# Kernel tuning notes

Measured on AMD Instinct MI355X. Metric: run time of the kernel, lower is better.

## Reference

```python
import jax, jax.numpy as jnp
import numpy as np

B, C, H, W = 4, 256, 64, 64
INTER = C // 2
BN_EPS = 1e-5


def setup_inputs() -> dict:
    key = jax.random.key(0)
    ks = jax.random.split(key, 12)
    s = 0.05
    return {
        "x": jax.random.normal(ks[0], (B, C, H, W), dtype=jnp.float32),
        "theta_w": jax.random.normal(ks[1], (INTER, C), dtype=jnp.float32) * s,
        "theta_b": jax.random.normal(ks[2], (INTER,), dtype=jnp.float32) * s,
        "phi_w": jax.random.normal(ks[3], (INTER, C), dtype=jnp.float32) * s,
        "phi_b": jax.random.normal(ks[4], (INTER,), dtype=jnp.float32) * s,
        "g_w": jax.random.normal(ks[5], (INTER, C), dtype=jnp.float32) * s,
        "g_b": jax.random.normal(ks[6], (INTER,), dtype=jnp.float32) * s,
        "W_w": jax.random.normal(ks[7], (C, INTER), dtype=jnp.float32) * s,
        "W_b": jax.random.normal(ks[8], (C,), dtype=jnp.float32) * s,
        "bn_gamma": jnp.ones((C,), dtype=jnp.float32),
        "bn_beta": jnp.zeros((C,), dtype=jnp.float32),
    }


def _conv1x1(x, w, b):
    # 1x1 conv == per-pixel GEMM: (B,C,H,W) x (O,C) -> (B,O,H,W)
    return jnp.einsum("bchw,oc->bohw", x, w) + b[None, :, None, None]


def reference(x, theta_w, theta_b, phi_w, phi_b, g_w, g_b, W_w, W_b, bn_gamma, bn_beta):
    b, c, h, w = x.shape
    hw = h * w
    theta = _conv1x1(x, theta_w, theta_b).reshape(b, -1, hw)  # (B, inter, HW) -> queries
    phi = _conv1x1(x, phi_w, phi_b).reshape(b, -1, hw)        # (B, inter, HW) -> keys
    g = _conv1x1(x, g_w, g_b).reshape(b, -1, hw)              # (B, inter, HW) -> values
    # f[n,m] = <theta[:,n], phi[:,m]> over all HW spatial positions
    f = jnp.einsum("bin,bim->bnm", theta, phi)                # (B, HW, HW)
    attn = jax.nn.softmax(f, axis=-1)
    y = jnp.einsum("bnm,bim->bin", attn, g)                   # (B, inter, HW)
    y = y.reshape(b, c // 2, h, w)
    wy = _conv1x1(y, W_w, W_b)                                # (B, C, H, W)
    # BatchNorm2d (training-mode batch statistics, per channel)
    mean = jnp.mean(wy, axis=(0, 2, 3), keepdims=True)
    var = jnp.var(wy, axis=(0, 2, 3), keepdims=True)
    wy_bn = bn_gamma[None, :, None, None] * (wy - mean) * jax.lax.rsqrt(var + BN_EPS) + bn_beta[None, :, None, None]
    return wy_bn + x
```

## Files before the change

kernel.cpp:

```cpp
#include <hip/hip_runtime.h>
#include <hip/hip_bf16.h>

#define HWN   4096
#define CIN   256
#define NINTER 128
#define NBATCH 4
#define BN_EPS 1e-5f
#define LOG2E 1.4426950408889634f
#define SMAX  64.0f

typedef __bf16 bf16_t;
typedef __bf16 bf16x8 __attribute__((ext_vector_type(8)));
typedef __bf16 bf16x4 __attribute__((ext_vector_type(4)));
typedef float  f32x4  __attribute__((ext_vector_type(4)));
typedef float  f32x16 __attribute__((ext_vector_type(16)));

__device__ __forceinline__ float fexp2(float x) {
  return __builtin_amdgcn_exp2f(x);
}

__device__ __forceinline__ void split_bf16(float v, bf16_t& h, bf16_t& l) {
  h = (bf16_t)v;
  l = (bf16_t)(v - (float)h);
}

__global__ __launch_bounds__(256) void convert_weights(
    const float* __restrict__ tw, const float* __restrict__ pw,
    const float* __restrict__ gw, const float* __restrict__ ww,
    bf16_t* __restrict__ out) {
  int i = blockIdx.x * 256 + threadIdx.x;
  float v;
  if (i < 32768)        v = tw[i];
  else if (i < 65536)   v = pw[i - 32768];
  else if (i < 98304)   v = gw[i - 65536];
  else                  v = ww[i - 98304];
  bf16_t h, l;
  split_bf16(v, h, l);
  out[i] = h;
  out[131072 + i] = l;
}

__global__ __launch_bounds__(256, 4) void qkv_kernel(
    const float* __restrict__ x, const bf16_t* __restrict__ wbf,
    const float* __restrict__ tb, const float* __restrict__ pb,
    const float* __restrict__ gb,
    bf16_t* __restrict__ Qh, bf16_t* __restrict__ Kh, bf16_t* __restrict__ V) {
  const int ntb  = blockIdx.x;
  const int b    = blockIdx.y;
  const int tid  = threadIdx.x;
  const int lane = tid & 63;
  const int wv   = tid >> 6;
  const int l31  = lane & 31;
  const int half = lane >> 5;

  __shared__ __align__(16) bf16_t smem[4608];
  bf16_t (*xTh)[72] = (bf16_t(*)[72])smem;
  bf16_t (*xTl)[72] = (bf16_t(*)[72])(smem + 2304);
  bf16_t (*Tr)[136] = (bf16_t(*)[136])smem;

  const bf16_t* Th = wbf;
  const bf16_t* Tl = wbf + 131072;
  const bf16_t* Ph = wbf + 32768;
  const bf16_t* Pl = wbf + 131072 + 32768;
  const bf16_t* Gh = wbf + 65536;
  const float*  xb = x + (size_t)b * CIN * HWN + ntb * 32;

  f32x16 aq, ak, av;
#pragma unroll
  for (int i = 0; i < 16; i++) { aq[i] = 0.f; ak[i] = 0.f; av[i] = 0.f; }

  for (int c0 = 0; c0 < 256; c0 += 64) {
    __syncthreads();
#pragma unroll
    for (int i = 0; i < 8; i++) {
      int idx = tid + i * 256;
      int cc = idx >> 5;
      int nn = idx & 31;
      float v = xb[(size_t)(c0 + cc) * HWN + nn];
      bf16_t h, l;
      split_bf16(v, h, l);
      xTh[nn][cc] = h;
      xTl[nn][cc] = l;
    }
    __syncthreads();
#pragma unroll
    for (int kk = 0; kk < 64; kk += 16) {
      size_t woff = (size_t)(32 * wv + l31) * 256 + c0 + kk + half * 8;
      bf16x8 th = *(const bf16x8*)(Th + woff);
      bf16x8 tl = *(const bf16x8*)(Tl + woff);
      bf16x8 ph = *(const bf16x8*)(Ph + woff);
      bf16x8 pl = *(const bf16x8*)(Pl + woff);
      bf16x8 gh = *(const bf16x8*)(Gh + woff);
      bf16x8 bh = *(const bf16x8*)(&xTh[l31][kk + half * 8]);
      bf16x8 bl = *(const bf16x8*)(&xTl[l31][kk + half * 8]);
      aq = __builtin_amdgcn_mfma_f32_32x32x16_bf16(th, bh, aq, 0, 0, 0);
      aq = __builtin_amdgcn_mfma_f32_32x32x16_bf16(th, bl, aq, 0, 0, 0);
      aq = __builtin_amdgcn_mfma_f32_32x32x16_bf16(tl, bh, aq, 0, 0, 0);
      ak = __builtin_amdgcn_mfma_f32_32x32x16_bf16(ph, bh, ak, 0, 0, 0);
      ak = __builtin_amdgcn_mfma_f32_32x32x16_bf16(ph, bl, ak, 0, 0, 0);
      ak = __builtin_amdgcn_mfma_f32_32x32x16_bf16(pl, bh, ak, 0, 0, 0);
      av = __builtin_amdgcn_mfma_f32_32x32x16_bf16(gh, bh, av, 0, 0, 0);
    }
  }

  const int trow = tid >> 3;
  const int tc16 = (tid & 7) * 16;
  bf16_t* qh = Qh + ((size_t)b * HWN + ntb * 32) * NINTER;
  bf16_t* kh = Kh + ((size_t)b * HWN + ntb * 32) * NINTER;

#pragma unroll
  for (int rnd = 0; rnd < 2; rnd++) {
    __syncthreads();
#pragma unroll
    for (int rg = 0; rg < 4; rg++) {
      int och0 = 32 * wv + 8 * rg + 4 * half;
#pragma unroll
      for (int j = 0; j < 4; j++) {
        float v = (rnd == 0) ? (aq[rg * 4 + j] + tb[och0 + j]) * LOG2E
                             : (ak[rg * 4 + j] + pb[och0 + j]);
        Tr[l31][och0 + j] = (bf16_t)v;
      }
    }
    __syncthreads();
    bf16_t* dst = (rnd == 0) ? qh : kh;
    bf16x8 v0 = *(const bf16x8*)(&Tr[trow][tc16]);
    bf16x8 v1 = *(const bf16x8*)(&Tr[trow][tc16 + 8]);
    *(bf16x8*)(dst + (size_t)trow * NINTER + tc16) = v0;
    *(bf16x8*)(dst + (size_t)trow * NINTER + tc16 + 8) = v1;
  }

  const int n = ntb * 32 + l31;
  bf16_t* vd = V + (size_t)b * NINTER * HWN;
#pragma unroll
  for (int r = 0; r < 16; r++) {
    int och = 32 * wv + (r & 3) + 8 * (r >> 2) + 4 * half;
    vd[(size_t)och * HWN + n] = (bf16_t)(av[r] + gb[och]);
  }
}

template<int NCv>
__global__ __launch_bounds__(256, 3) void attn_kernel(
    const bf16_t* __restrict__ Qh, const bf16_t* __restrict__ Kh,
    const bf16_t* __restrict__ V,
    float* __restrict__ Opart, float* __restrict__ Lp) {
  constexpr int CH = HWN / NCv;
  constexpr int NT = CH / 32;
  const int qt    = blockIdx.x;
  const int chunk = blockIdx.y;
  const int b     = blockIdx.z;
  const int tid   = threadIdx.x;
  const int lane  = tid & 63;
  const int wv    = tid >> 6;
  const int l15   = lane & 15;
  const int quad  = lane >> 4;
  const int kbase = chunk * CH;

  __shared__ __align__(16) bf16_t Klds[32][136];
  __shared__ __align__(16) bf16_t Vlds[144][56];
  __shared__ __align__(16) bf16_t Plds[4][32][40];

  const bf16_t* Qhb = Qh + (size_t)b * HWN * NINTER;
  const bf16_t* Khb = Kh + (size_t)b * HWN * NINTER;
  const bf16_t* Vb  = V + (size_t)b * NINTER * HWN;

  if (tid < 112) {
    int row = 128 + tid / 7;
    int c8 = (tid % 7) * 8;
    bf16x8 v;
#pragma unroll
    for (int j = 0; j < 8; j++) v[j] = (bf16_t)((row == 128) ? 1.0f : 0.0f);
    *(bf16x8*)(&Vlds[row][c8]) = v;
  }

  bf16x8 qf[2][4];
#pragma unroll
  for (int qs = 0; qs < 2; qs++) {
    const int qrow = qt * 128 + wv * 32 + qs * 16 + l15;
#pragma unroll
    for (int kc = 0; kc < 4; kc++)
      qf[qs][kc] = *(const bf16x8*)(Qhb + (size_t)qrow * NINTER + kc * 32 + quad * 8);
  }

  f32x4 o[2][8], ol[2];
#pragma unroll
  for (int qs = 0; qs < 2; qs++) {
#pragma unroll
    for (int dt = 0; dt < 8; dt++)
#pragma unroll
      for (int i = 0; i < 4; i++) o[qs][dt][i] = 0.f;
#pragma unroll
    for (int i = 0; i < 4; i++) ol[qs][i] = 0.f;
  }

  auto load_tile = [&](uint4* kr, uint4* vr, int t) {
#pragma unroll
    for (int i = 0; i < 2; i++) {
      int idx = tid + i * 256;
      kr[i] = *(const uint4*)(Khb + (size_t)(kbase + t * 32 + (idx >> 4)) * NINTER + (idx & 15) * 8);
    }
#pragma unroll
    for (int i = 0; i < 2; i++) {
      int idx = tid + i * 256;
      vr[i] = *(const uint4*)(Vb + (size_t)(idx >> 2) * HWN + kbase + t * 32 + (idx & 3) * 8);
    }
  };
  auto store_tile = [&](const uint4* kr, const uint4* vr) {
#pragma unroll
    for (int i = 0; i < 2; i++) {
      int idx = tid + i * 256;
      *(uint4*)(&Klds[idx >> 4][(idx & 15) * 8]) = kr[i];
    }
#pragma unroll
    for (int i = 0; i < 2; i++) {
      int idx = tid + i * 256;
      *(uint4*)(&Vlds[idx >> 2][(idx & 3) * 8]) = vr[i];
    }
  };

  auto compute = [&]() {
    f32x4 s[2][2];
#pragma unroll
    for (int qs = 0; qs < 2; qs++)
#pragma unroll
      for (int ks = 0; ks < 2; ks++)
#pragma unroll
        for (int i = 0; i < 4; i++) s[qs][ks][i] = 0.f;
#pragma unroll
    for (int ks = 0; ks < 2; ks++)
#pragma unroll
      for (int kc = 0; kc < 4; kc++) {
        bf16x8 kf = *(const bf16x8*)(&Klds[ks * 16 + l15][kc * 32 + quad * 8]);
        s[0][ks] = __builtin_amdgcn_mfma_f32_16x16x32_bf16(kf, qf[0][kc], s[0][ks], 0, 0, 0);
        s[1][ks] = __builtin_amdgcn_mfma_f32_16x16x32_bf16(kf, qf[1][kc], s[1][ks], 0, 0, 0);
      }

#pragma unroll
    for (int qs = 0; qs < 2; qs++)
#pragma unroll
      for (int ks = 0; ks < 2; ks++) {
        bf16x4 p4;
#pragma unroll
        for (int r = 0; r < 4; r++)
          p4[r] = (bf16_t)fexp2(s[qs][ks][r] - SMAX);
        *(bf16x4*)(&Plds[wv][qs * 16 + l15][ks * 16 + quad * 4]) = p4;
      }

    bf16x8 pf0 = *(const bf16x8*)(&Plds[wv][l15][quad * 8]);
    bf16x8 pf1 = *(const bf16x8*)(&Plds[wv][16 + l15][quad * 8]);
#pragma unroll
    for (int dt = 0; dt < 8; dt++) {
      bf16x8 vf = *(const bf16x8*)(&Vlds[dt * 16 + l15][quad * 8]);
      o[0][dt] = __builtin_amdgcn_mfma_f32_16x16x32_bf16(pf0, vf, o[0][dt], 0, 0, 0);
      o[1][dt] = __builtin_amdgcn_mfma_f32_16x16x32_bf16(pf1, vf, o[1][dt], 0, 0, 0);
    }
    bf16x8 vfl = *(const bf16x8*)(&Vlds[128 + l15][quad * 8]);
    ol[0] = __builtin_amdgcn_mfma_f32_16x16x32_bf16(pf0, vfl, ol[0], 0, 0, 0);
    ol[1] = __builtin_amdgcn_mfma_f32_16x16x32_bf16(pf1, vfl, ol[1], 0, 0, 0);
  };

  uint4 krA[2], vrA[2], krB[2], vrB[2];
  load_tile(krA, vrA, 0);

#pragma unroll 1
  for (int t = 0; t < NT; t += 2) {
    __builtin_amdgcn_s_barrier();
    __builtin_amdgcn_sched_barrier(0);
    store_tile(krA, vrA);
    __builtin_amdgcn_sched_barrier(0);
    load_tile(krB, vrB, t + 1);
    __builtin_amdgcn_sched_barrier(0);
    asm volatile("s_waitcnt lgkmcnt(0)" ::: "memory");
    __builtin_amdgcn_sched_barrier(0);
    __builtin_amdgcn_s_barrier();
    __builtin_amdgcn_sched_barrier(0);
    compute();

    __builtin_amdgcn_s_barrier();
    __builtin_amdgcn_sched_barrier(0);
    store_tile(krB, vrB);
    __builtin_amdgcn_sched_barrier(0);
    if (t + 2 < NT) load_tile(krA, vrA, t + 2);
    __builtin_amdgcn_sched_barrier(0);
    asm volatile("s_waitcnt lgkmcnt(0)" ::: "memory");
    __builtin_amdgcn_sched_barrier(0);
    __builtin_amdgcn_s_barrier();
    __builtin_amdgcn_sched_barrier(0);
    compute();
  }

  float* Ob = Opart + ((size_t)(b * NCv + chunk) * HWN) * NINTER;
#pragma unroll
  for (int qs = 0; qs < 2; qs++)
#pragma unroll
    for (int r = 0; r < 4; r++) {
      int n = qt * 128 + wv * 32 + qs * 16 + quad * 4 + r;
#pragma unroll
      for (int dt = 0; dt < 8; dt++)
        Ob[(size_t)n * NINTER + dt * 16 + l15] = o[qs][dt][r];
      if (l15 == 0)
        Lp[(size_t)(b * NCv + chunk) * HWN + n] = ol[qs][r];
    }
}

template<int NCv>
__global__ __launch_bounds__(256, 4) void wconv_kernel(
    const bf16_t* __restrict__ Wbf, const float* __restrict__ Opart,
    const float* __restrict__ Lp, const float* __restrict__ Wb,
    bf16_t* __restrict__ WY) {
  const int ntb = blockIdx.x;
  const int b   = blockIdx.y;
  const int tid = threadIdx.x;
  const int lane = tid & 63;
  const int wv   = tid >> 6;
  const int l31  = lane & 31;
  const int half = lane >> 5;

  __shared__ __align__(16) bf16_t Ylds[32][136];
  __shared__ float Linv[32];

  if (tid < 32) {
    int n = ntb * 32 + tid;
    float ls = 0.f;
#pragma unroll
    for (int c = 0; c < NCv; c++) ls += Lp[(size_t)(b * NCv + c) * HWN + n];
    Linv[tid] = 1.f / ls;
  }

  const int nrow = tid >> 3;
  const int dgrp = tid & 7;
  float oacc[16];
#pragma unroll
  for (int j = 0; j < 16; j++) oacc[j] = 0.f;
#pragma unroll
  for (int c = 0; c < NCv; c++) {
    const float* Op = Opart +
        ((size_t)(b * NCv + c) * HWN + ntb * 32 + nrow) * NINTER + dgrp * 16;
#pragma unroll
    for (int q = 0; q < 4; q++) {
      f32x4 v = *(const f32x4*)(Op + q * 4);
#pragma unroll
      for (int j = 0; j < 4; j++) oacc[q * 4 + j] += v[j];
    }
  }
  __syncthreads();
  {
    float inv = Linv[nrow];
    bf16x8 y0, y1;
#pragma unroll
    for (int j = 0; j < 8; j++) {
      y0[j] = (bf16_t)(oacc[j] * inv);
      y1[j] = (bf16_t)(oacc[8 + j] * inv);
    }
    *(bf16x8*)(&Ylds[nrow][dgrp * 16]) = y0;
    *(bf16x8*)(&Ylds[nrow][dgrp * 16 + 8]) = y1;
  }
  __syncthreads();

  const bf16_t* Wh = Wbf + 98304;
  f32x16 acc[2];
#pragma unroll
  for (int c = 0; c < 2; c++)
#pragma unroll
    for (int i = 0; i < 16; i++) acc[c][i] = 0.f;

#pragma unroll
  for (int k0 = 0; k0 < 128; k0 += 16) {
    bf16x8 a0 = *(const bf16x8*)(Wh + (size_t)(wv * 64 + l31) * NINTER + k0 + half * 8);
    bf16x8 a1 = *(const bf16x8*)(Wh + (size_t)(wv * 64 + 32 + l31) * NINTER + k0 + half * 8);
    bf16x8 b0 = *(const bf16x8*)(&Ylds[l31][k0 + half * 8]);
    acc[0] = __builtin_amdgcn_mfma_f32_32x32x16_bf16(a0, b0, acc[0], 0, 0, 0);
    acc[1] = __builtin_amdgcn_mfma_f32_32x32x16_bf16(a1, b0, acc[1], 0, 0, 0);
  }

  bf16_t* dst = WY + (size_t)b * 256 * HWN + ntb * 32;
#pragma unroll
  for (int ct = 0; ct < 2; ct++)
#pragma unroll
    for (int r = 0; r < 16; r++) {
      int co = wv * 64 + ct * 32 + (r & 3) + 8 * (r >> 2) + 4 * half;
      dst[(size_t)co * HWN + l31] = (bf16_t)(acc[ct][r] + Wb[co]);
    }
}

__global__ __launch_bounds__(256) void stats_kernel(
    const bf16_t* __restrict__ WY, float* __restrict__ stats) {
  const int c = blockIdx.x;
  const int tid = threadIdx.x;
  float s = 0.f, s2 = 0.f;
  for (int b = 0; b < NBATCH; b++) {
    const bf16_t* p = WY + ((size_t)b * 256 + c) * HWN;
    for (int i = tid * 8; i < HWN; i += 2048) {
      bf16x8 v8 = *(const bf16x8*)(p + i);
#pragma unroll
      for (int j = 0; j < 8; j++) {
        float v = (float)v8[j];
        s += v;
        s2 += v * v;
      }
    }
  }
#pragma unroll
  for (int off = 1; off < 64; off <<= 1) {
    s += __shfl_xor(s, off);
    s2 += __shfl_xor(s2, off);
  }
  __shared__ float red[8];
  int wv = tid >> 6;
  if ((tid & 63) == 0) { red[wv] = s; red[4 + wv] = s2; }
  __syncthreads();
  if (tid == 0) {
    float S = red[0] + red[1] + red[2] + red[3];
    float S2 = red[4] + red[5] + red[6] + red[7];
    float mean = S * (1.f / 16384.f);
    float var = S2 * (1.f / 16384.f) - mean * mean;
    stats[c] = mean;
    stats[256 + c] = rsqrtf(var + BN_EPS);
  }
}

__global__ __launch_bounds__(256) void bn_kernel(
    const bf16_t* __restrict__ WY, const float* __restrict__ x,
    const float* __restrict__ stats, const float* __restrict__ gamma,
    const float* __restrict__ beta, float* __restrict__ out) {
  int idx = blockIdx.x * 256 + threadIdx.x;
  int e = idx * 4;
  int c = (e >> 12) & 255;
  bf16x4 w4 = *(const bf16x4*)(WY + e);
  float4 xv = *(const float4*)(x + e);
  float mean = stats[c];
  float g = gamma[c] * stats[256 + c];
  float bb = beta[c];
  float4 o;
  o.x = g * ((float)w4[0] - mean) + bb + xv.x;
  o.y = g * ((float)w4[1] - mean) + bb + xv.y;
  o.z = g * ((float)w4[2] - mean) + bb + xv.z;
  o.w = g * ((float)w4[3] - mean) + bb + xv.w;
  *(float4*)(out + e) = o;
}

extern "C" void kernel_launch(void* const* d_in, const int* in_sizes, int n_in,
                              void* d_out, int out_size, void* d_ws, size_t ws_size,
                              hipStream_t stream) {
  const float* x       = (const float*)d_in[0];
  const float* theta_b = (const float*)d_in[2];
  const float* phi_b   = (const float*)d_in[4];
  const float* g_b     = (const float*)d_in[6];
  const float* W_b     = (const float*)d_in[8];
  const float* bn_g    = (const float*)d_in[9];
  const float* bn_b    = (const float*)d_in[10];
  float* out = (float*)d_out;

  const size_t NEED8 = 12582912ull + 67108864ull + 8388608ull + 524288ull +
                       524288ull + 2048ull;
  const int nc = (ws_size >= NEED8) ? 8 : 4;
  const size_t opb = (size_t)nc * HWN * NINTER * NBATCH * 4;
  const size_t lpb = (size_t)nc * HWN * NBATCH * 4;

  char* ws = (char*)d_ws;
  bf16_t* Qh  = (bf16_t*)(ws);
  bf16_t* Kh  = (bf16_t*)(ws + 4194304);
  bf16_t* V   = (bf16_t*)(ws + 8388608);
  float*  OP  = (float*)(ws + 12582912);
  bf16_t* WY  = (bf16_t*)(ws + 12582912 + opb);
  float*  LP  = (float*)(ws + 12582912 + opb + 8388608);
  bf16_t* WBF = (bf16_t*)(ws + 12582912 + opb + 8388608 + lpb);
  float*  ST  = (float*)(ws + 12582912 + opb + 8388608 + lpb + 524288);

  convert_weights<<<512, 256, 0, stream>>>(
      (const float*)d_in[1], (const float*)d_in[3],
      (const float*)d_in[5], (const float*)d_in[7], WBF);
  qkv_kernel<<<dim3(128, NBATCH), 256, 0, stream>>>(
      x, WBF, theta_b, phi_b, g_b, Qh, Kh, V);
  if (nc == 8) {
    attn_kernel<8><<<dim3(32, 8, NBATCH), 256, 0, stream>>>(Qh, Kh, V, OP, LP);
    wconv_kernel<8><<<dim3(128, NBATCH), 256, 0, stream>>>(WBF, OP, LP, W_b, WY);
  } else {
    attn_kernel<4><<<dim3(32, 4, NBATCH), 256, 0, stream>>>(Qh, Kh, V, OP, LP);
    wconv_kernel<4><<<dim3(128, NBATCH), 256, 0, stream>>>(WBF, OP, LP, W_b, WY);
  }
  stats_kernel<<<256, 256, 0, stream>>>(WY, ST);
  bn_kernel<<<4096, 256, 0, stream>>>(WY, x, ST, bn_g, bn_b, out);
}
```

Before: 209.8 us.

## Double query tile per attention block and drop register-prefetch pipeline

Each attention block now handles 256 queries (64 per wave) instead of 128, so every K/V tile staged in shared memory is reused across twice as many MFMA ops and total K/V global traffic is halved. The grid is halved to match and launch bounds are lowered to 2 blocks per CU to make room for the larger accumulator set. The manual double-buffered register prefetch with sched_barriers is replaced by a simple synchronous load-sync-compute loop. This risks exposing global load latency and lowers occupancy, with fewer blocks to fill the GPU.

Result: faster. 195.6 us (-6.8%).

```diff
diff --git a/kernel.cpp b/kernel.cpp
--- a/kernel.cpp
+++ b/kernel.cpp
@@ -139,7 +139,7 @@
 }
 
 template<int NCv>
-__global__ __launch_bounds__(256, 3) void attn_kernel(
+__global__ __launch_bounds__(256, 2) void attn_kernel(
     const bf16_t* __restrict__ Qh, const bf16_t* __restrict__ Kh,
     const bf16_t* __restrict__ V,
     float* __restrict__ Opart, float* __restrict__ Lp) {
@@ -157,7 +157,7 @@
 
   __shared__ __align__(16) bf16_t Klds[32][136];
   __shared__ __align__(16) bf16_t Vlds[144][56];
-  __shared__ __align__(16) bf16_t Plds[4][32][40];
+  __shared__ __align__(16) bf16_t Plds[4][64][40];
 
   const bf16_t* Qhb = Qh + (size_t)b * HWN * NINTER;
   const bf16_t* Khb = Kh + (size_t)b * HWN * NINTER;
@@ -172,18 +172,18 @@
     *(bf16x8*)(&Vlds[row][c8]) = v;
   }
 
-  bf16x8 qf[2][4];
-#pragma unroll
-  for (int qs = 0; qs < 2; qs++) {
-    const int qrow = qt * 128 + wv * 32 + qs * 16 + l15;
+  bf16x8 qf[4][4];
+#pragma unroll
+  for (int qs = 0; qs < 4; qs++) {
+    const int qrow = qt * 256 + wv * 64 + qs * 16 + l15;
 #pragma unroll
     for (int kc = 0; kc < 4; kc++)
       qf[qs][kc] = *(const bf16x8*)(Qhb + (size_t)qrow * NINTER + kc * 32 + quad * 8);
   }
 
-  f32x4 o[2][8], ol[2];
-#pragma unroll
-  for (int qs = 0; qs < 2; qs++) {
+  f32x4 o[4][8], ol[4];
+#pragma unroll
+  for (int qs = 0; qs < 4; qs++) {
 #pragma unroll
     for (int dt = 0; dt < 8; dt++)
 #pragma unroll
@@ -192,108 +192,73 @@
     for (int i = 0; i < 4; i++) ol[qs][i] = 0.f;
   }
 
-  auto load_tile = [&](uint4* kr, uint4* vr, int t) {
+  for (int t = 0; t < NT; t++) {
+    __syncthreads();
 #pragma unroll
     for (int i = 0; i < 2; i++) {
       int idx = tid + i * 256;
-      kr[i] = *(const uint4*)(Khb + (size_t)(kbase + t * 32 + (idx >> 4)) * NINTER + (idx & 15) * 8);
+      int row = idx >> 4;
+      int c8 = (idx & 15) * 8;
+      *(uint4*)(&Klds[row][c8]) =
+          *(const uint4*)(Khb + (size_t)(kbase + t * 32 + row) * NINTER + c8);
     }
 #pragma unroll
     for (int i = 0; i < 2; i++) {
       int idx = tid + i * 256;
-      vr[i] = *(const uint4*)(Vb + (size_t)(idx >> 2) * HWN + kbase + t * 32 + (idx & 3) * 8);
-    }
-  };
-  auto store_tile = [&](const uint4* kr, const uint4* vr) {
-#pragma unroll
-    for (int i = 0; i < 2; i++) {
-      int idx = tid + i * 256;
-      *(uint4*)(&Klds[idx >> 4][(idx & 15) * 8]) = kr[i];
-    }
-#pragma unroll
-    for (int i = 0; i < 2; i++) {
-      int idx = tid + i * 256;
-      *(uint4*)(&Vlds[idx >> 2][(idx & 3) * 8]) = vr[i];
-    }
-  };
-
-  auto compute = [&]() {
-    f32x4 s[2][2];
-#pragma unroll
-    for (int qs = 0; qs < 2; qs++)
-#pragma unroll
-      for (int ks = 0; ks < 2; ks++)
-#pragma unroll
-        for (int i = 0; i < 4; i++) s[qs][ks][i] = 0.f;
-#pragma unroll
-    for (int ks = 0; ks < 2; ks++)
+      int row = idx >> 2;
+      int c8 = (idx & 3) * 8;
+      *(uint4*)(&Vlds[row][c8]) =
+          *(const uint4*)(Vb + (size_t)row * HWN + kbase + t * 32 + c8);
+    }
+    __syncthreads();
+
+#pragma unroll
+    for (int ks = 0; ks < 2; ks++) {
+      f32x4 s4[4];
+#pragma unroll
+      for (int qs = 0; qs < 4; qs++)
+#pragma unroll
+        for (int i = 0; i < 4; i++) s4[qs][i] = 0.f;
 #pragma unroll
       for (int kc = 0; kc < 4; kc++) {
         bf16x8 kf = *(const bf16x8*)(&Klds[ks * 16 + l15][kc * 32 + quad * 8]);
-        s[0][ks] = __builtin_amdgcn_mfma_f32_16x16x32_bf16(kf, qf[0][kc], s[0][ks], 0, 0, 0);
-        s[1][ks] = __builtin_amdgcn_mfma_f32_16x16x32_bf16(kf, qf[1][kc], s[1][ks], 0, 0, 0);
+#pragma unroll
+        for (int qs = 0; qs < 4; qs++)
+          s4[qs] = __builtin_amdgcn_mfma_f32_16x16x32_bf16(kf, qf[qs][kc], s4[qs], 0, 0, 0);
       }
-
-#pragma unroll
-    for (int qs = 0; qs < 2; qs++)
-#pragma unroll
-      for (int ks = 0; ks < 2; ks++) {
+#pragma unroll
+      for (int qs = 0; qs < 4; qs++) {
         bf16x4 p4;
 #pragma unroll
         for (int r = 0; r < 4; r++)
-          p4[r] = (bf16_t)fexp2(s[qs][ks][r] - SMAX);
+          p4[r] = (bf16_t)fexp2(s4[qs][r] - SMAX);
         *(bf16x4*)(&Plds[wv][qs * 16 + l15][ks * 16 + quad * 4]) = p4;
       }
-
-    bf16x8 pf0 = *(const bf16x8*)(&Plds[wv][l15][quad * 8]);
-    bf16x8 pf1 = *(const bf16x8*)(&Plds[wv][16 + l15][quad * 8]);
+    }
+
+    bf16x8 pf[4];
+#pragma unroll
+    for (int qs = 0; qs < 4; qs++)
+      pf[qs] = *(const bf16x8*)(&Plds[wv][qs * 16 + l15][quad * 8]);
 #pragma unroll
     for (int dt = 0; dt < 8; dt++) {
       bf16x8 vf = *(const bf16x8*)(&Vlds[dt * 16 + l15][quad * 8]);
-      o[0][dt] = __builtin_amdgcn_mfma_f32_16x16x32_bf16(pf0, vf, o[0][dt], 0, 0, 0);
-      o[1][dt] = __builtin_amdgcn_mfma_f32_16x16x32_bf16(pf1, vf, o[1][dt], 0, 0, 0);
+#pragma unroll
+      for (int qs = 0; qs < 4; qs++)
+        o[qs][dt] = __builtin_amdgcn_mfma_f32_16x16x32_bf16(pf[qs], vf, o[qs][dt], 0, 0, 0);
     }
     bf16x8 vfl = *(const bf16x8*)(&Vlds[128 + l15][quad * 8]);
-    ol[0] = __builtin_amdgcn_mfma_f32_16x16x32_bf16(pf0, vfl, ol[0], 0, 0, 0);
-    ol[1] = __builtin_amdgcn_mfma_f32_16x16x32_bf16(pf1, vfl, ol[1], 0, 0, 0);
-  };
-
-  uint4 krA[2], vrA[2], krB[2], vrB[2];
-  load_tile(krA, vrA, 0);
-
-#pragma unroll 1
-  for (int t = 0; t < NT; t += 2) {
-    __builtin_amdgcn_s_barrier();
-    __builtin_amdgcn_sched_barrier(0);
-    store_tile(krA, vrA);
-    __builtin_amdgcn_sched_barrier(0);
-    load_tile(krB, vrB, t + 1);
-    __builtin_amdgcn_sched_barrier(0);
-    asm volatile("s_waitcnt lgkmcnt(0)" ::: "memory");
-    __builtin_amdgcn_sched_barrier(0);
-    __builtin_amdgcn_s_barrier();
-    __builtin_amdgcn_sched_barrier(0);
-    compute();
-
-    __builtin_amdgcn_s_barrier();
-    __builtin_amdgcn_sched_barrier(0);
-    store_tile(krB, vrB);
-    __builtin_amdgcn_sched_barrier(0);
-    if (t + 2 < NT) load_tile(krA, vrA, t + 2);
-    __builtin_amdgcn_sched_barrier(0);
-    asm volatile("s_waitcnt lgkmcnt(0)" ::: "memory");
-    __builtin_amdgcn_sched_barrier(0);
-    __builtin_amdgcn_s_barrier();
-    __builtin_amdgcn_sched_barrier(0);
-    compute();
+#pragma unroll
+    for (int qs = 0; qs < 4; qs++)
+      ol[qs] = __builtin_amdgcn_mfma_f32_16x16x32_bf16(pf[qs], vfl, ol[qs], 0, 0, 0);
   }
 
   float* Ob = Opart + ((size_t)(b * NCv + chunk) * HWN) * NINTER;
 #pragma unroll
-  for (int qs = 0; qs < 2; qs++)
+  for (int qs = 0; qs < 4; qs++)
 #pragma unroll
     for (int r = 0; r < 4; r++) {
-      int n = qt * 128 + wv * 32 + qs * 16 + quad * 4 + r;
+      int n = qt * 256 + wv * 64 + qs * 16 + quad * 4 + r;
 #pragma unroll
       for (int dt = 0; dt < 8; dt++)
         Ob[(size_t)n * NINTER + dt * 16 + l15] = o[qs][dt][r];
@@ -472,10 +437,10 @@
   qkv_kernel<<<dim3(128, NBATCH), 256, 0, stream>>>(
       x, WBF, theta_b, phi_b, g_b, Qh, Kh, V);
   if (nc == 8) {
-    attn_kernel<8><<<dim3(32, 8, NBATCH), 256, 0, stream>>>(Qh, Kh, V, OP, LP);
+    attn_kernel<8><<<dim3(16, 8, NBATCH), 256, 0, stream>>>(Qh, Kh, V, OP, LP);
     wconv_kernel<8><<<dim3(128, NBATCH), 256, 0, stream>>>(WBF, OP, LP, W_b, WY);
   } else {
-    attn_kernel<4><<<dim3(32, 4, NBATCH), 256, 0, stream>>>(Qh, Kh, V, OP, LP);
+    attn_kernel<4><<<dim3(16, 4, NBATCH), 256, 0, stream>>>(Qh, Kh, V, OP, LP);
     wconv_kernel<4><<<dim3(128, NBATCH), 256, 0, stream>>>(WBF, OP, LP, W_b, WY);
   }
   stats_kernel<<<256, 256, 0, stream>>>(WY, ST);
```
